# Performance work log

Hardware: AMD Instinct MI355X
Metric: run time of the kernel (lower is better)

The kernel has to match this reference:

```python
import jax, jax.numpy as jnp
import numpy as np

N = 8192      # nodes
E = 16384     # edges
G = 512       # graphs
IN = 235      # node feature dim (input_dim)
H = 64        # hidden_dim
ED = 52       # edge feature dim


def setup_inputs() -> dict:
    key = jax.random.key(0)
    ks = jax.random.split(key, 24)
    s = lambda fan_in: 1.0 / np.sqrt(fan_in)
    inp = {}
    inp["x"] = jax.random.normal(ks[0], (N, IN), dtype=jnp.float32)
    inp["edge_index"] = jax.random.randint(ks[1], (2, E), 0, N)
    inp["edge_attr"] = jax.random.uniform(ks[2], (E, ED), dtype=jnp.float32)
    inp["batch"] = jnp.sort(jax.random.randint(ks[3], (N,), 0, G))
    # EdgeModel (nn of nnconv1): Linear(52,128) -> Linear(128, 235*64)
    inp["W1"] = jax.random.normal(ks[4], (128, ED), dtype=jnp.float32) * s(ED)
    inp["b1"] = jnp.zeros((128,), jnp.float32)
    inp["W2"] = jax.random.normal(ks[5], (IN * H, 128), dtype=jnp.float32) * s(128)
    inp["b2"] = jnp.zeros((IN * H,), jnp.float32)
    # NNConv root weight and bias
    inp["root"] = jax.random.normal(ks[6], (IN, H), dtype=jnp.float32) * s(IN)
    inp["conv_b"] = jnp.zeros((H,), jnp.float32)
    # MLP head
    inp["fw1"] = jax.random.normal(ks[7], (128, H), dtype=jnp.float32) * s(H)
    inp["fb1"] = jnp.zeros((128,), jnp.float32)
    inp["fw2"] = jax.random.normal(ks[8], (256, 128), dtype=jnp.float32) * s(128)
    inp["fb2"] = jnp.zeros((256,), jnp.float32)
    inp["fw3"] = jax.random.normal(ks[9], (128, 256), dtype=jnp.float32) * s(256)
    inp["fb3"] = jnp.zeros((128,), jnp.float32)
    inp["fw4"] = jax.random.normal(ks[10], (1, 128), dtype=jnp.float32) * s(128)
    inp["fb4"] = jnp.zeros((1,), jnp.float32)
    return inp


def reference(x, edge_index, edge_attr, batch, W1, b1, W2, b2, root, conv_b,
              fw1, fb1, fw2, fb2, fw3, fb3, fw4, fb4):
    src, dst = edge_index[0], edge_index[1]
    # edge MLP -> per-edge weight matrices [E, IN, H]
    h = edge_attr @ W1.T + b1
    w = (h @ W2.T + b2).reshape(E, IN, H)
    # gather source node feats, per-edge matmul, scatter-add to destinations
    msg = jnp.einsum('ei,eih->eh', x[src], w)          # [E, H]
    agg = jax.ops.segment_sum(msg, dst, num_segments=N)  # [N, H]
    out = jax.nn.relu(agg + x @ root + conv_b)           # NNConv + ReLU
    # global mean pool per graph
    summ = jax.ops.segment_sum(out, batch, num_segments=G)
    cnt = jax.ops.segment_sum(jnp.ones((N, 1), out.dtype), batch, num_segments=G)
    pooled = summ / jnp.maximum(cnt, 1.0)                # [G, H]
    # dense MLP head
    y = jax.nn.relu(pooled @ fw1.T + fb1)
    y = jax.nn.relu(y @ fw2.T + fb2)
    y = jax.nn.relu(y @ fw3.T + fb3)
    return y @ fw4.T + fb4                               # [G, 1]
```

## Files before the change

### kernel.cpp

```cpp
#include <hip/hip_runtime.h>
#include <hip/hip_bf16.h>
#include <stdint.h>

#define N_NODES 8192
#define N_EDGES 16384
#define N_GRAPHS 512
#define IN_DIM 235
#define H_DIM 64
#define ED_DIM 52
#define HID1 128
#define KP 256
#define NB 3328
#define NBE 3456

typedef __bf16 bf16x8 __attribute__((ext_vector_type(8)));
typedef float f32x4 __attribute__((ext_vector_type(4)));

static __device__ inline unsigned short f2bf(float f) {
    union { float f; unsigned u; } v; v.f = f;
    unsigned r = v.u + 0x7FFFu + ((v.u >> 16) & 1u);
    return (unsigned short)(r >> 16);
}
static __device__ inline float bf2f(unsigned short s) {
    union { unsigned u; float f; } v; v.u = ((unsigned)s) << 16;
    return v.f;
}

__global__ __launch_bounds__(256) void k_build_bt(const float* __restrict__ W1,
                                                  const float* __restrict__ W2,
                                                  unsigned short* __restrict__ Bt) {
    __shared__ float w1s[HID1 * ED_DIM];
    __shared__ float w2s[64 * 129];
    const int i = blockIdx.x;
    const int t = threadIdx.x;
    for (int j = t; j < HID1 * ED_DIM; j += 256) w1s[j] = W1[j];
    const float* w2src = W2 + (size_t)i * 64 * HID1;
    for (int j = t; j < 64 * HID1; j += 256) w2s[(j >> 7) * 129 + (j & 127)] = w2src[j];
    __syncthreads();
    for (int p = t; p < NB; p += 256) {
        const int d = p >> 6, h = p & 63;
        float acc = 0.f;
        #pragma unroll 8
        for (int k = 0; k < HID1; ++k)
            acc += w1s[k * ED_DIM + d] * w2s[h * 129 + k];
        Bt[(size_t)p * KP + i] = f2bf(acc);
    }
}

__global__ __launch_bounds__(256) void k_build_bc(const float* __restrict__ W2,
                                                  const float* __restrict__ b1,
                                                  const float* __restrict__ b2,
                                                  float* __restrict__ bc) {
    const int j = blockIdx.x * 256 + threadIdx.x;
    if (j >= IN_DIM * H_DIM) return;
    float acc = b2[j];
    const float* w = W2 + (size_t)j * HID1;
    #pragma unroll 8
    for (int k = 0; k < HID1; ++k) acc += w[k] * b1[k];
    bc[j] = acc;
}

__global__ __launch_bounds__(256) void k_build_ext(const float* __restrict__ root,
                                                   const float* __restrict__ bc,
                                                   unsigned short* __restrict__ Bt) {
    const int j = blockIdx.x;
    const int i = threadIdx.x;
    if (i >= IN_DIM) return;
    const float v = (j < 64) ? root[i * H_DIM + j] : bc[i * H_DIM + (j - 64)];
    Bt[(size_t)(NB + j) * KP + i] = f2bf(v);
}

__global__ __launch_bounds__(256) void k_build_a(const float* __restrict__ x,
                                                 unsigned short* __restrict__ A) {
    const int j = blockIdx.x * 256 + threadIdx.x;
    const int n = j >> 8, i = j & 255;
    A[j] = (i < IN_DIM) ? f2bf(x[n * IN_DIM + i]) : (unsigned short)0;
}

__global__ __launch_bounds__(256) void k_gemm(const unsigned short* __restrict__ A,
                                              const unsigned short* __restrict__ Bt,
                                              unsigned short* __restrict__ P,
                                              float* __restrict__ agg,
                                              float* __restrict__ xb2,
                                              const float* __restrict__ conv_b) {
    __shared__ unsigned short As[128 * 32];
    __shared__ unsigned short Bs[128 * 32];
    const int t = threadIdx.x;
    const int m0 = blockIdx.y * 128, n0 = blockIdx.x * 128;
    const int wid = t >> 6, lane = t & 63;
    const int wm = wid >> 1, wn = wid & 1;
    const int q = lane >> 4, r16 = lane & 15;

    f32x4 acc[4][4] = {};

    for (int k0 = 0; k0 < KP; k0 += 32) {
        __syncthreads();
        #pragma unroll
        for (int r = 0; r < 2; ++r) {
            const int idx = r * 256 + t;
            const int row = idx >> 2, col = (idx & 3) * 8;
            const unsigned short* ga = &A[(size_t)(m0 + row) * KP + k0 + col];
            const unsigned short* gb = &Bt[(size_t)(n0 + row) * KP + k0 + col];
            char* la = (char*)As + r * 4096 + wid * 1024;
            char* lb = (char*)Bs + r * 4096 + wid * 1024;
            __builtin_amdgcn_global_load_lds(
                (const __attribute__((address_space(1))) unsigned int*)ga,
                (__attribute__((address_space(3))) unsigned int*)la, 16, 0, 0);
            __builtin_amdgcn_global_load_lds(
                (const __attribute__((address_space(1))) unsigned int*)gb,
                (__attribute__((address_space(3))) unsigned int*)lb, 16, 0, 0);
        }
        __syncthreads();
        bf16x8 af[4], bfr[4];
        #pragma unroll
        for (int mi = 0; mi < 4; ++mi)
            af[mi] = *(const bf16x8*)(&As[(wm * 64 + mi * 16 + r16) * 32 + q * 8]);
        #pragma unroll
        for (int ni = 0; ni < 4; ++ni)
            bfr[ni] = *(const bf16x8*)(&Bs[(wn * 64 + ni * 16 + r16) * 32 + q * 8]);
        #pragma unroll
        for (int mi = 0; mi < 4; ++mi)
            #pragma unroll
            for (int ni = 0; ni < 4; ++ni)
                acc[mi][ni] = __builtin_amdgcn_mfma_f32_16x16x32_bf16(
                    af[mi], bfr[ni], acc[mi][ni], 0, 0, 0);
    }

    #pragma unroll
    for (int mi = 0; mi < 4; ++mi)
        #pragma unroll
        for (int ni = 0; ni < 4; ++ni) {
            const int c = n0 + wn * 64 + ni * 16 + r16;
            #pragma unroll
            for (int rr = 0; rr < 4; ++rr) {
                const int row = m0 + wm * 64 + mi * 16 + q * 4 + rr;
                const float v = acc[mi][ni][rr];
                if (c < NB) {
                    P[(size_t)row * NB + c] = f2bf(v);
                } else if (c < NB + 64) {
                    agg[row * H_DIM + (c - NB)] = v + conv_b[c - NB];
                } else {
                    xb2[row * H_DIM + (c - NB - 64)] = v;
                }
            }
        }
}

__global__ __launch_bounds__(256) void k_edge(const int* __restrict__ ei,
                                              const float* __restrict__ ea,
                                              const unsigned short* __restrict__ P,
                                              const float* __restrict__ xb2,
                                              float* __restrict__ agg) {
    const int e = (blockIdx.x * 256 + threadIdx.x) >> 6;
    const int h = threadIdx.x & 63;
    if (e >= N_EDGES) return;
    const int s = ei[e], dst = ei[N_EDGES + e];
    const unsigned short* Pr = P + (size_t)s * NB;
    const float* ear = ea + (size_t)e * ED_DIM;
    float acc = xb2[s * H_DIM + h];
    #pragma unroll 4
    for (int d = 0; d < ED_DIM; ++d)
        acc += ear[d] * bf2f(Pr[d * H_DIM + h]);
    atomicAdd(&agg[dst * H_DIM + h], acc);
}

__global__ __launch_bounds__(256) void k_pool(const float* __restrict__ agg,
                                              const int* __restrict__ batch,
                                              float* __restrict__ psum,
                                              float* __restrict__ pcnt) {
    const int n = (blockIdx.x * 256 + threadIdx.x) >> 6;
    const int h = threadIdx.x & 63;
    if (n >= N_NODES) return;
    const float v = fmaxf(agg[n * H_DIM + h], 0.f);
    const int g = batch[n];
    atomicAdd(&psum[g * H_DIM + h], v);
    if (h == 0) atomicAdd(&pcnt[g], 1.0f);
}

__global__ __launch_bounds__(256) void k_head(const float* __restrict__ psum,
                                              const float* __restrict__ pcnt,
                                              const float* __restrict__ fw1, const float* __restrict__ fb1,
                                              const float* __restrict__ fw2, const float* __restrict__ fb2,
                                              const float* __restrict__ fw3, const float* __restrict__ fb3,
                                              const float* __restrict__ fw4, const float* __restrict__ fb4,
                                              float* __restrict__ out) {
    __shared__ float sp[64], s1[128], s2[256], s3[128];
    const int g = blockIdx.x, t = threadIdx.x;
    if (t < 64) sp[t] = psum[g * 64 + t] / fmaxf(pcnt[g], 1.0f);
    __syncthreads();
    if (t < 128) {
        float a = fb1[t];
        const float* w = fw1 + t * 64;
        #pragma unroll 8
        for (int k = 0; k < 64; ++k) a += sp[k] * w[k];
        s1[t] = fmaxf(a, 0.f);
    }
    __syncthreads();
    {
        float a = fb2[t];
        const float* w = fw2 + t * 128;
        #pragma unroll 8
        for (int k = 0; k < 128; ++k) a += s1[k] * w[k];
        s2[t] = fmaxf(a, 0.f);
    }
    __syncthreads();
    if (t < 128) {
        float a = fb3[t];
        const float* w = fw3 + t * 256;
        #pragma unroll 8
        for (int k = 0; k < 256; ++k) a += s2[k] * w[k];
        s3[t] = fmaxf(a, 0.f);
    }
    __syncthreads();
    if (t < 64) {
        float p = s3[t] * fw4[t] + s3[t + 64] * fw4[t + 64];
        #pragma unroll
        for (int off = 32; off > 0; off >>= 1) p += __shfl_down(p, off);
        if (t == 0) out[g] = p + fb4[0];
    }
}

extern "C" void kernel_launch(void* const* d_in, const int* in_sizes, int n_in,
                              void* d_out, int out_size, void* d_ws, size_t ws_size,
                              hipStream_t stream) {
    const float* x      = (const float*)d_in[0];
    const int*   ei     = (const int*)d_in[1];
    const float* ea     = (const float*)d_in[2];
    const int*   batch  = (const int*)d_in[3];
    const float* W1     = (const float*)d_in[4];
    const float* b1     = (const float*)d_in[5];
    const float* W2     = (const float*)d_in[6];
    const float* b2     = (const float*)d_in[7];
    const float* root   = (const float*)d_in[8];
    const float* conv_b = (const float*)d_in[9];
    const float* fw1 = (const float*)d_in[10]; const float* fb1 = (const float*)d_in[11];
    const float* fw2 = (const float*)d_in[12]; const float* fb2 = (const float*)d_in[13];
    const float* fw3 = (const float*)d_in[14]; const float* fb3 = (const float*)d_in[15];
    const float* fw4 = (const float*)d_in[16]; const float* fb4 = (const float*)d_in[17];
    float* out = (float*)d_out;

    char* ws = (char*)d_ws;
    unsigned short* A   = (unsigned short*)(ws);
    unsigned short* Bt  = (unsigned short*)(ws + 4194304);
    unsigned short* P   = (unsigned short*)(ws + 5963776);
    float* agg  = (float*)(ws + 60489728);
    float* xb2  = (float*)(ws + 62586880);
    float* bc   = (float*)(ws + 64684032);
    float* psum = (float*)(ws + 64744192);
    float* pcnt = (float*)(ws + 64875264);

    hipMemsetAsync(Bt, 0, (size_t)NBE * KP * sizeof(unsigned short), stream);
    hipMemsetAsync(psum, 0, (size_t)(N_GRAPHS * H_DIM + N_GRAPHS) * sizeof(float), stream);

    k_build_bc<<<dim3((IN_DIM * H_DIM + 255) / 256), dim3(256), 0, stream>>>(W2, b1, b2, bc);
    k_build_bt<<<dim3(IN_DIM), dim3(256), 0, stream>>>(W1, W2, Bt);
    k_build_ext<<<dim3(128), dim3(256), 0, stream>>>(root, bc, Bt);
    k_build_a<<<dim3(N_NODES), dim3(256), 0, stream>>>(x, A);
    k_gemm<<<dim3(NBE / 128, N_NODES / 128), dim3(256), 0, stream>>>(A, Bt, P, agg, xb2, conv_b);
    k_edge<<<dim3(N_EDGES / 4), dim3(256), 0, stream>>>(ei, ea, P, xb2, agg);
    k_pool<<<dim3(N_NODES / 4), dim3(256), 0, stream>>>(agg, batch, psum, pcnt);
    k_head<<<dim3(N_GRAPHS), dim3(256), 0, stream>>>(psum, pcnt, fw1, fb1, fw2, fb2, fw3, fb3, fw4, fb4, out);
}
```

Baseline: 219.8 us.

## Swizzle GEMM LDS tiles, vectorize epilogue stores, split weight-fold kernel across blocks

The GEMM now XOR-swizzles the 16-byte column groups of its LDS tiles to reduce bank conflicts on fragment reads. It also swaps the MFMA operands so each lane holds four consecutive output columns, which lets the epilogue write packed bf16 and float4 stores instead of scattered scalar ones. The weight-folding kernel k_build_bt is split across four blocks per column, with a transposed W1 slice and float4 dot products, to add parallelism and cut per-block work. The risk is in the swizzle and transposed-output index math, which must match exactly, and the column ranges must stay aligned to the 128-wide tile split.

```diff
diff --git a/kernel.cpp b/kernel.cpp
--- a/kernel.cpp
+++ b/kernel.cpp
@@ -29,20 +29,30 @@
 __global__ __launch_bounds__(256) void k_build_bt(const float* __restrict__ W1,
                                                   const float* __restrict__ W2,
                                                   unsigned short* __restrict__ Bt) {
-    __shared__ float w1s[HID1 * ED_DIM];
-    __shared__ float w2s[64 * 129];
+    __shared__ float w1s[13 * HID1];
+    __shared__ float w2s[64 * 132];
     const int i = blockIdx.x;
+    const int by = blockIdx.y;
     const int t = threadIdx.x;
-    for (int j = t; j < HID1 * ED_DIM; j += 256) w1s[j] = W1[j];
+    const int dbase = by * 13;
+    for (int j = t; j < 13 * HID1; j += 256) {
+        const int dd = j >> 7, k = j & 127;
+        w1s[j] = W1[k * ED_DIM + dbase + dd];
+    }
     const float* w2src = W2 + (size_t)i * 64 * HID1;
-    for (int j = t; j < 64 * HID1; j += 256) w2s[(j >> 7) * 129 + (j & 127)] = w2src[j];
-    __syncthreads();
-    for (int p = t; p < NB; p += 256) {
-        const int d = p >> 6, h = p & 63;
+    for (int j = t; j < 64 * HID1; j += 256) w2s[(j >> 7) * 132 + (j & 127)] = w2src[j];
+    __syncthreads();
+    const int pend = by * 832 + 832;
+    for (int p = by * 832 + t; p < pend; p += 256) {
+        const int dd = (p >> 6) - dbase, h = p & 63;
+        const float4* w1v = (const float4*)&w1s[dd * HID1];
+        const float4* w2v = (const float4*)&w2s[h * 132];
         float acc = 0.f;
-        #pragma unroll 8
-        for (int k = 0; k < HID1; ++k)
-            acc += w1s[k * ED_DIM + d] * w2s[h * 129 + k];
+        #pragma unroll
+        for (int k4 = 0; k4 < HID1 / 4; ++k4) {
+            const float4 a = w1v[k4], b = w2v[k4];
+            acc += a.x * b.x + a.y * b.y + a.z * b.z + a.w * b.w;
+        }
         Bt[(size_t)p * KP + i] = f2bf(acc);
     }
 }
@@ -98,9 +108,10 @@
         #pragma unroll
         for (int r = 0; r < 2; ++r) {
             const int idx = r * 256 + t;
-            const int row = idx >> 2, col = (idx & 3) * 8;
-            const unsigned short* ga = &A[(size_t)(m0 + row) * KP + k0 + col];
-            const unsigned short* gb = &Bt[(size_t)(n0 + row) * KP + k0 + col];
+            const int row = idx >> 2;
+            const int lgrp = (((idx & 3) ^ ((row >> 1) & 3))) * 8;
+            const unsigned short* ga = &A[(size_t)(m0 + row) * KP + k0 + lgrp];
+            const unsigned short* gb = &Bt[(size_t)(n0 + row) * KP + k0 + lgrp];
             char* la = (char*)As + r * 4096 + wid * 1024;
             char* lb = (char*)Bs + r * 4096 + wid * 1024;
             __builtin_amdgcn_global_load_lds(
@@ -112,38 +123,54 @@
         }
         __syncthreads();
         bf16x8 af[4], bfr[4];
-        #pragma unroll
-        for (int mi = 0; mi < 4; ++mi)
-            af[mi] = *(const bf16x8*)(&As[(wm * 64 + mi * 16 + r16) * 32 + q * 8]);
+        const int pcq = (q ^ ((r16 >> 1) & 3)) * 8;
+        #pragma unroll
+        for (int mi = 0; mi < 4; ++mi)
+            af[mi] = *(const bf16x8*)(&As[(wm * 64 + mi * 16 + r16) * 32 + pcq]);
         #pragma unroll
         for (int ni = 0; ni < 4; ++ni)
-            bfr[ni] = *(const bf16x8*)(&Bs[(wn * 64 + ni * 16 + r16) * 32 + q * 8]);
+            bfr[ni] = *(const bf16x8*)(&Bs[(wn * 64 + ni * 16 + r16) * 32 + pcq]);
         #pragma unroll
         for (int mi = 0; mi < 4; ++mi)
             #pragma unroll
             for (int ni = 0; ni < 4; ++ni)
                 acc[mi][ni] = __builtin_amdgcn_mfma_f32_16x16x32_bf16(
-                    af[mi], bfr[ni], acc[mi][ni], 0, 0, 0);
-    }
-
-    #pragma unroll
-    for (int mi = 0; mi < 4; ++mi)
-        #pragma unroll
-        for (int ni = 0; ni < 4; ++ni) {
-            const int c = n0 + wn * 64 + ni * 16 + r16;
+                    bfr[ni], af[mi], acc[mi][ni], 0, 0, 0);
+    }
+
+    if (n0 < NB) {
+        #pragma unroll
+        for (int mi = 0; mi < 4; ++mi)
             #pragma unroll
-            for (int rr = 0; rr < 4; ++rr) {
-                const int row = m0 + wm * 64 + mi * 16 + q * 4 + rr;
-                const float v = acc[mi][ni][rr];
-                if (c < NB) {
-                    P[(size_t)row * NB + c] = f2bf(v);
-                } else if (c < NB + 64) {
-                    agg[row * H_DIM + (c - NB)] = v + conv_b[c - NB];
+            for (int ni = 0; ni < 4; ++ni) {
+                const int row = m0 + wm * 64 + mi * 16 + r16;
+                const int col = n0 + wn * 64 + ni * 16 + q * 4;
+                union { unsigned short us[4]; uint2 u2; } pk;
+                #pragma unroll
+                for (int rr = 0; rr < 4; ++rr) pk.us[rr] = f2bf(acc[mi][ni][rr]);
+                *(uint2*)(&P[(size_t)row * NB + col]) = pk.u2;
+            }
+    } else {
+        #pragma unroll
+        for (int mi = 0; mi < 4; ++mi)
+            #pragma unroll
+            for (int ni = 0; ni < 4; ++ni) {
+                const int row = m0 + wm * 64 + mi * 16 + r16;
+                const int cl = ni * 16 + q * 4;
+                if (wn == 0) {
+                    const float4 cb = *(const float4*)&conv_b[cl];
+                    float4 v;
+                    v.x = acc[mi][ni][0] + cb.x; v.y = acc[mi][ni][1] + cb.y;
+                    v.z = acc[mi][ni][2] + cb.z; v.w = acc[mi][ni][3] + cb.w;
+                    *(float4*)(&agg[row * H_DIM + cl]) = v;
                 } else {
-                    xb2[row * H_DIM + (c - NB - 64)] = v;
+                    float4 v;
+                    v.x = acc[mi][ni][0]; v.y = acc[mi][ni][1];
+                    v.z = acc[mi][ni][2]; v.w = acc[mi][ni][3];
+                    *(float4*)(&xb2[row * H_DIM + cl]) = v;
                 }
             }
-        }
+    }
 }
 
 __global__ __launch_bounds__(256) void k_edge(const int* __restrict__ ei,
@@ -253,7 +280,7 @@
     hipMemsetAsync(psum, 0, (size_t)(N_GRAPHS * H_DIM + N_GRAPHS) * sizeof(float), stream);
 
     k_build_bc<<<dim3((IN_DIM * H_DIM + 255) / 256), dim3(256), 0, stream>>>(W2, b1, b2, bc);
-    k_build_bt<<<dim3(IN_DIM), dim3(256), 0, stream>>>(W1, W2, Bt);
+    k_build_bt<<<dim3(IN_DIM, 4), dim3(256), 0, stream>>>(W1, W2, Bt);
     k_build_ext<<<dim3(128), dim3(256), 0, stream>>>(root, bc, Bt);
     k_build_a<<<dim3(N_NODES), dim3(256), 0, stream>>>(x, A);
     k_gemm<<<dim3(NBE / 128, N_NODES / 128), dim3(256), 0, stream>>>(A, Bt, P, agg, xb2, conv_b);
```

Result: slower. 225.9 us (+2.8%).
